# Kernel tuning notes

Measured on AMD Instinct MI355X. Metric: run time of the kernel, lower is better.

## Reference

```python
import jax, jax.numpy as jnp
import numpy as np

B, T, C = 4, 2048, 1024
H = 16
HD = C // H  # 64


def setup_inputs() -> dict:
    key = jax.random.key(0)
    k1, k2, k3 = jax.random.split(key, 3)
    x = jax.random.normal(k1, (B, T, C), dtype=jnp.float32)
    W_attn = jax.random.normal(k2, (C, 3 * C), dtype=jnp.float32) * (1.0 / np.sqrt(C))
    b_attn = jnp.zeros((3 * C,), dtype=jnp.float32)
    W_proj = jax.random.normal(k3, (C, C), dtype=jnp.float32) * (1.0 / np.sqrt(C))
    b_proj = jnp.zeros((C,), dtype=jnp.float32)
    return {"x": x, "W_attn": W_attn, "b_attn": b_attn, "W_proj": W_proj, "b_proj": b_proj}


def reference(x, W_attn, b_attn, W_proj, b_proj):
    Bx, Tx, Cx = x.shape
    qkv = x @ W_attn + b_attn                      # [B,T,3C]
    q, k, v = jnp.split(qkv, 3, axis=-1)
    # [B,T,C] -> [B,H,T,HD]
    q = q.reshape(Bx, Tx, H, HD).transpose(0, 2, 1, 3)
    k = k.reshape(Bx, Tx, H, HD).transpose(0, 2, 1, 3)
    v = v.reshape(Bx, Tx, H, HD).transpose(0, 2, 1, 3)
    att = jnp.einsum('bhqd,bhkd->bhqk', q, k) / jnp.sqrt(jnp.float32(HD))
    causal = jnp.tril(jnp.ones((Tx, Tx), dtype=bool))
    att = jnp.where(causal[None, None], att, -jnp.inf)
    att = jax.nn.softmax(att, axis=-1)
    y = jnp.einsum('bhqk,bhkd->bhqd', att, v)      # [B,H,T,HD]
    y = y.transpose(0, 2, 1, 3).reshape(Bx, Tx, Cx)
    return y @ W_proj + b_proj
```

## Files before the change

### kernel.cpp

```cpp
#include <hip/hip_runtime.h>
#include <hip/hip_bf16.h>

typedef unsigned short u16;
typedef __attribute__((ext_vector_type(8))) short bf16x8;
typedef __attribute__((ext_vector_type(4))) float f32x4;

#define MFMA16(a, b, c) __builtin_amdgcn_mfma_f32_16x16x32_bf16((a), (b), (c), 0, 0, 0)

__device__ __forceinline__ u16 f2bf(float f) {
  union { float f; unsigned u; } v; v.f = f;
  unsigned r = v.u + 0x7fffu + ((v.u >> 16) & 1u);
  return (u16)(r >> 16);
}

__device__ __forceinline__ unsigned pk_trunc(float hi, float lo) {
  union { float f; unsigned u; } a, b; a.f = hi; b.f = lo;
  return __builtin_amdgcn_perm(a.u, b.u, 0x07060302u);
}

__device__ __forceinline__ void gload_lds16(const u16* g, u16* l) {
  __builtin_amdgcn_global_load_lds((const __attribute__((address_space(1))) void*)g,
                                   (__attribute__((address_space(3))) void*)l, 16, 0, 0);
}

__global__ __launch_bounds__(256) void convert_bf16_k(const float* __restrict__ in,
                                                      u16* __restrict__ out, int n) {
  int i = (blockIdx.x * 256 + threadIdx.x) * 4;
  if (i >= n) return;
  float4 v = *(const float4*)(in + i);
  ushort4 o;
  o.x = f2bf(v.x); o.y = f2bf(v.y); o.z = f2bf(v.z); o.w = f2bf(v.w);
  *(ushort4*)(out + i) = o;
}

__global__ __launch_bounds__(256) void transpose2_k(const float* __restrict__ Wa, u16* __restrict__ WaT,
                                                    const float* __restrict__ Wp, u16* __restrict__ WpT) {
  __shared__ float tile[64][65];
  int b = blockIdx.x;
  const float* W; u16* Wt; int N, n0, k0;
  if (b < 768) { W = Wa; Wt = WaT; N = 3072; n0 = (b % 48) * 64; k0 = (b / 48) * 64; }
  else { int c = b - 768; W = Wp; Wt = WpT; N = 1024; n0 = (c & 15) * 64; k0 = (c >> 4) * 64; }
  const int tx = threadIdx.x & 63, ty = threadIdx.x >> 6;
#pragma unroll
  for (int i = 0; i < 16; ++i)
    tile[ty + 4 * i][tx] = W[(size_t)(k0 + ty + 4 * i) * N + n0 + tx];
  __syncthreads();
#pragma unroll
  for (int i = 0; i < 16; ++i)
    Wt[(size_t)(n0 + ty + 4 * i) * 1024 + k0 + tx] = f2bf(tile[tx][ty + 4 * i]);
}

#define GEMM_PROLOG                                                                \
  __shared__ u16 As[128 * 32];                                                     \
  __shared__ u16 Bs[128 * 32];                                                     \
  const int tid = threadIdx.x;                                                     \
  const int w = tid >> 6, lane = tid & 63;                                         \
  const int wm = w & 1, wn = w >> 1;                                               \
  const int fr = lane & 15, fg = lane >> 4;                                        \
  const int srow = lane >> 2, skof = (lane & 3) * 8;                               \
  u16* lA = As + w * 1024;                                                         \
  u16* lB = Bs + w * 1024;                                                         \
  f32x4 acc[4][4];                                                                 \
  _Pragma("unroll") for (int i = 0; i < 4; i++)                                    \
      _Pragma("unroll") for (int j = 0; j < 4; j++) acc[i][j] = (f32x4){0, 0, 0, 0};

#define GEMM_KLOOP(Aptr, Btptr, SWAP)                                              \
  {                                                                                \
    const u16* gA0 = (Aptr) + (size_t)(m0 + w * 32 + srow) * 1024 + skof;          \
    const u16* gB0 = (Btptr) + (size_t)(n0 + w * 32 + srow) * 1024 + skof;         \
    for (int kt = 0; kt < 32; ++kt) {                                              \
      const int ko = kt * 32;                                                      \
      gload_lds16(gA0 + ko, lA);                                                   \
      gload_lds16(gA0 + ko + 16 * 1024, lA + 512);                                 \
      gload_lds16(gB0 + ko, lB);                                                   \
      gload_lds16(gB0 + ko + 16 * 1024, lB + 512);                                 \
      __syncthreads();                                                             \
      bf16x8 af[4], bfr[4];                                                        \
      _Pragma("unroll") for (int mb = 0; mb < 4; ++mb)                             \
          af[mb] = *(const bf16x8*)&As[(wm * 64 + mb * 16 + fr) * 32 + fg * 8];    \
      _Pragma("unroll") for (int nb = 0; nb < 4; ++nb)                             \
          bfr[nb] = *(const bf16x8*)&Bs[(wn * 64 + nb * 16 + fr) * 32 + fg * 8];   \
      _Pragma("unroll") for (int mb = 0; mb < 4; ++mb)                             \
          _Pragma("unroll") for (int nb = 0; nb < 4; ++nb)                         \
              acc[mb][nb] = (SWAP) ? MFMA16(bfr[nb], af[mb], acc[mb][nb])          \
                                   : MFMA16(af[mb], bfr[nb], acc[mb][nb]);         \
      __syncthreads();                                                             \
    }                                                                              \
  }

__global__ __launch_bounds__(256) void gemm_qkv(const u16* __restrict__ A,
                                                const u16* __restrict__ Bt,
                                                const float* __restrict__ bias,
                                                u16* __restrict__ Qo, u16* __restrict__ Ko,
                                                u16* __restrict__ Vt) {
  const int id = blockIdx.x;
  const int s = id >> 3;
  const int nt = (id & 7) * 3 + s % 3;
  const int mt = s / 3;
  const int m0 = mt * 128, n0 = nt * 128;
  GEMM_PROLOG
  const int which = n0 >> 10;
  if (which < 2) {
    GEMM_KLOOP(A, Bt, 1)
    const float sc = (which == 0) ? 0.125f : 1.0f;
    u16* Out = (which == 0) ? Qo : Ko;
#pragma unroll
    for (int mb = 0; mb < 4; ++mb) {
      const int tg = m0 + wm * 64 + mb * 16 + fr;
      const int bb = tg >> 11, t = tg & 2047;
#pragma unroll
      for (int nb = 0; nb < 4; ++nb) {
        const int n = n0 + wn * 64 + nb * 16 + 4 * fg;
        const float4 b4 = *(const float4*)(bias + n);
        const int c = n & 1023, h = c >> 6, d0 = c & 63;
        const float v0 = (acc[mb][nb][0] + b4.x) * sc;
        const float v1 = (acc[mb][nb][1] + b4.y) * sc;
        const float v2 = (acc[mb][nb][2] + b4.z) * sc;
        const float v3 = (acc[mb][nb][3] + b4.w) * sc;
        const unsigned lo = (unsigned)f2bf(v0) | ((unsigned)f2bf(v1) << 16);
        const unsigned hi = (unsigned)f2bf(v2) | ((unsigned)f2bf(v3) << 16);
        *(uint2*)(Out + ((size_t)(bb * 16 + h) * 2048 + t) * 64 + d0) = make_uint2(lo, hi);
      }
    }
  } else {
    GEMM_KLOOP(A, Bt, 0)
#pragma unroll
    for (int nb = 0; nb < 4; ++nb) {
      const int n = n0 + wn * 64 + nb * 16 + fr;
      const float bs = bias[n];
      const int c = n & 1023, h = c >> 6, hd = c & 63;
#pragma unroll
      for (int mb = 0; mb < 4; ++mb) {
        const int mbase = m0 + wm * 64 + mb * 16 + fg * 4;
        const int bb = mbase >> 11, t = mbase & 2047;
        ushort4 pv;
        pv.x = f2bf(acc[mb][nb][0] + bs);
        pv.y = f2bf(acc[mb][nb][1] + bs);
        pv.z = f2bf(acc[mb][nb][2] + bs);
        pv.w = f2bf(acc[mb][nb][3] + bs);
        *(ushort4*)(Vt + ((size_t)(bb * 16 + h) * 64 + hd) * 2048 + t) = pv;
      }
    }
  }
}

__global__ __launch_bounds__(256) void gemm_proj(const u16* __restrict__ A,
                                                 const u16* __restrict__ Bt,
                                                 const float* __restrict__ bias,
                                                 float* __restrict__ O) {
  const int id = blockIdx.x;
  const int m0 = (id >> 3) * 128, n0 = (id & 7) * 128;
  GEMM_PROLOG
  GEMM_KLOOP(A, Bt, 1)
#pragma unroll
  for (int mb = 0; mb < 4; ++mb) {
    const int tg = m0 + wm * 64 + mb * 16 + fr;
#pragma unroll
    for (int nb = 0; nb < 4; ++nb) {
      const int n = n0 + wn * 64 + nb * 16 + 4 * fg;
      const float4 b4 = *(const float4*)(bias + n);
      float4 o;
      o.x = acc[mb][nb][0] + b4.x;
      o.y = acc[mb][nb][1] + b4.y;
      o.z = acc[mb][nb][2] + b4.z;
      o.w = acc[mb][nb][3] + b4.w;
      *(float4*)(O + (size_t)tg * 1024 + n) = o;
    }
  }
}

#define PSTR 72
__global__ __launch_bounds__(256) void attn_k(const u16* __restrict__ Q,
                                              const u16* __restrict__ Kb,
                                              const u16* __restrict__ Vt,
                                              u16* __restrict__ Y) {
  __shared__ u16 Ks[64 * 72];
  __shared__ u16 Vs[64 * 72];
  __shared__ u16 Ps[4 * 32 * PSTR];
  const int L = blockIdx.x;
  const int xcd = L & 7, slot = L >> 3;
  const int bh = xcd * 8 + (slot & 7);
  const int qt = 15 - (slot >> 3);
  const int tid = threadIdx.x, w = tid >> 6, lane = tid & 63;
  const int fr = lane & 15, fg = lane >> 4;
  const u16* Qp = Q + (size_t)bh * 2048 * 64;
  const u16* Kp = Kb + (size_t)bh * 2048 * 64;
  const u16* Vp = Vt + (size_t)bh * 64 * 2048;
  const int qw = qt * 128 + w * 32;

  bf16x8 qa[2][2];
#pragma unroll
  for (int g = 0; g < 2; ++g)
#pragma unroll
    for (int c = 0; c < 2; ++c)
      qa[g][c] = *(const bf16x8*)(Qp + (size_t)(qw + g * 16 + fr) * 64 + c * 32 + fg * 8);

  float li[2] = {0.f, 0.f};
  f32x4 ot[2][4];
#pragma unroll
  for (int g = 0; g < 2; ++g)
#pragma unroll
    for (int mb = 0; mb < 4; ++mb) ot[g][mb] = (f32x4){0, 0, 0, 0};

  const int srow = tid >> 2, scol = (tid & 3) * 16;
  u16* Pw = Ps + w * 32 * PSTR;
  const int nk = 2 * qt + 2;
  const u16* Kg = Kp + (size_t)srow * 64 + scol;
  const u16* Vg = Vp + (size_t)srow * 2048 + scol;

  uint4 kr0 = *(const uint4*)(Kg);
  uint4 kr1 = *(const uint4*)(Kg + 8);
  uint4 vr0 = *(const uint4*)(Vg);
  uint4 vr1 = *(const uint4*)(Vg + 8);

  for (int jt = 0; jt < nk; ++jt) {
    const int k0 = jt * 64;
    if (jt) __syncthreads();
    *(uint4*)&Ks[srow * 72 + scol] = kr0;
    *(uint4*)&Ks[srow * 72 + scol + 8] = kr1;
    *(uint4*)&Vs[srow * 72 + scol] = vr0;
    *(uint4*)&Vs[srow * 72 + scol + 8] = vr1;
    __syncthreads();
    if (jt + 1 < nk) {
      const int kn = (jt + 1) * 64;
      kr0 = *(const uint4*)(Kg + (size_t)kn * 64);
      kr1 = *(const uint4*)(Kg + (size_t)kn * 64 + 8);
      vr0 = *(const uint4*)(Vg + kn);
      vr1 = *(const uint4*)(Vg + kn + 8);
    }
    if (k0 > qw + 31) continue;

    bf16x8 kb[4][2];
#pragma unroll
    for (int nb = 0; nb < 4; ++nb) {
      kb[nb][0] = *(const bf16x8*)&Ks[(nb * 16 + fr) * 72 + fg * 8];
      kb[nb][1] = *(const bf16x8*)&Ks[(nb * 16 + fr) * 72 + 32 + fg * 8];
    }
    f32x4 st[2][4];
#pragma unroll
    for (int g = 0; g < 2; ++g)
#pragma unroll
      for (int nb = 0; nb < 4; ++nb) {
        f32x4 z = (f32x4){0, 0, 0, 0};
        z = MFMA16(kb[nb][0], qa[g][0], z);
        z = MFMA16(kb[nb][1], qa[g][1], z);
        st[g][nb] = z;
      }
    const bool needmask = (k0 + 63 > qw);
#pragma unroll
    for (int g = 0; g < 2; ++g) {
      const int q = qw + g * 16 + fr;
      float rs0 = 0.f, rs1 = 0.f;
#pragma unroll
      for (int nb = 0; nb < 4; ++nb) {
        const int kcb = k0 + nb * 16 + 4 * fg;
        float p0 = __expf(st[g][nb][0]);
        float p1 = __expf(st[g][nb][1]);
        float p2 = __expf(st[g][nb][2]);
        float p3 = __expf(st[g][nb][3]);
        if (needmask) {
          p0 = (kcb + 0 > q) ? 0.f : p0;
          p1 = (kcb + 1 > q) ? 0.f : p1;
          p2 = (kcb + 2 > q) ? 0.f : p2;
          p3 = (kcb + 3 > q) ? 0.f : p3;
        }
        rs0 += p0 + p1;
        rs1 += p2 + p3;
        *(uint2*)&Pw[(g * 16 + fr) * PSTR + nb * 16 + 4 * fg] =
            make_uint2(pk_trunc(p1, p0), pk_trunc(p3, p2));
      }
      li[g] += rs0 + rs1;
    }
    bf16x8 pa[2][2];
#pragma unroll
    for (int g = 0; g < 2; ++g)
#pragma unroll
      for (int H = 0; H < 2; ++H)
        pa[g][H] = *(const bf16x8*)&Pw[(g * 16 + fr) * PSTR + H * 32 + fg * 8];
#pragma unroll
    for (int mb = 0; mb < 4; ++mb) {
      bf16x8 vb0 = *(const bf16x8*)&Vs[(mb * 16 + fr) * 72 + fg * 8];
      bf16x8 vb1 = *(const bf16x8*)&Vs[(mb * 16 + fr) * 72 + 32 + fg * 8];
#pragma unroll
      for (int g = 0; g < 2; ++g) {
        ot[g][mb] = MFMA16(vb0, pa[g][0], ot[g][mb]);
        ot[g][mb] = MFMA16(vb1, pa[g][1], ot[g][mb]);
      }
    }
  }

  const int b = bh >> 4, h = bh & 15;
#pragma unroll
  for (int g = 0; g < 2; ++g) {
    float l = li[g];
    l += __shfl_xor(l, 16);
    l += __shfl_xor(l, 32);
    const float inv = 1.0f / l;
    const int t = qw + g * 16 + fr;
    u16* yrow = Y + ((size_t)b * 2048 + t) * 1024 + h * 64;
#pragma unroll
    for (int mb = 0; mb < 4; ++mb) {
      const unsigned d0 = (unsigned)f2bf(ot[g][mb][0] * inv) |
                          ((unsigned)f2bf(ot[g][mb][1] * inv) << 16);
      const unsigned d1 = (unsigned)f2bf(ot[g][mb][2] * inv) |
                          ((unsigned)f2bf(ot[g][mb][3] * inv) << 16);
      *(uint2*)&yrow[mb * 16 + fg * 4] = make_uint2(d0, d1);
    }
  }
}

extern "C" void kernel_launch(void* const* d_in, const int* in_sizes, int n_in,
                              void* d_out, int out_size, void* d_ws, size_t ws_size,
                              hipStream_t stream) {
  const float* x = (const float*)d_in[0];
  const float* Wa = (const float*)d_in[1];
  const float* ba = (const float*)d_in[2];
  const float* Wp = (const float*)d_in[3];
  const float* bp = (const float*)d_in[4];
  float* out = (float*)d_out;

  char* p = (char*)d_ws;
  u16* xb = (u16*)p;   p += (size_t)8192 * 1024 * 2;
  u16* WaT = (u16*)p;  p += (size_t)3072 * 1024 * 2;
  u16* WpT = (u16*)p;  p += (size_t)1024 * 1024 * 2;
  u16* Qb = (u16*)p;   p += (size_t)64 * 2048 * 64 * 2;
  u16* Kbuf = (u16*)p; p += (size_t)64 * 2048 * 64 * 2;
  u16* Vtb = (u16*)p;  p += (size_t)64 * 64 * 2048 * 2;
  u16* Yb = (u16*)p;   p += (size_t)8192 * 1024 * 2;

  convert_bf16_k<<<8192, 256, 0, stream>>>(x, xb, 8192 * 1024);
  transpose2_k<<<1024, 256, 0, stream>>>(Wa, WaT, Wp, WpT);
  gemm_qkv<<<1536, 256, 0, stream>>>(xb, WaT, ba, Qb, Kbuf, Vtb);
  attn_k<<<1024, 256, 0, stream>>>(Qb, Kbuf, Vtb, Yb);
  gemm_proj<<<512, 256, 0, stream>>>(Yb, WpT, bp, out);
}
```

Measured before the change: 271.7 us.

## Double attention query tile per block and simplify QKV GEMM epilogue and grid

The attention kernel now gives each wave 64 query rows (256 per block) instead of 32, so every K/V tile staged in shared memory is reused across twice as many queries, and the grid is halved to 512 blocks. The QKV GEMM drops the XCD-aware block swizzle in favour of a plain 2D grid, and uses a single non-swapped MFMA order with scalar strided stores for Q and K. The goal is to cut K/V reload traffic and barrier overhead per query. In exchange, register pressure rises (more accumulators), there are fewer blocks for load balance on the causal triangle, and the Q/K stores become uncoalesced 2-byte writes.

```diff
diff --git a/kernel.cpp b/kernel.cpp
--- a/kernel.cpp
+++ b/kernel.cpp
@@ -93,46 +93,29 @@
                                                 const float* __restrict__ bias,
                                                 u16* __restrict__ Qo, u16* __restrict__ Ko,
                                                 u16* __restrict__ Vt) {
-  const int id = blockIdx.x;
-  const int s = id >> 3;
-  const int nt = (id & 7) * 3 + s % 3;
-  const int mt = s / 3;
-  const int m0 = mt * 128, n0 = nt * 128;
+  const int m0 = blockIdx.y * 128, n0 = blockIdx.x * 128;
   GEMM_PROLOG
+  GEMM_KLOOP(A, Bt, 0)
   const int which = n0 >> 10;
-  if (which < 2) {
-    GEMM_KLOOP(A, Bt, 1)
-    const float sc = (which == 0) ? 0.125f : 1.0f;
-    u16* Out = (which == 0) ? Qo : Ko;
+#pragma unroll
+  for (int nb = 0; nb < 4; ++nb) {
+    const int n = n0 + wn * 64 + nb * 16 + fr;
+    const float bs = bias[n];
+    const int c = n & 1023, h = c >> 6, hd = c & 63;
 #pragma unroll
     for (int mb = 0; mb < 4; ++mb) {
-      const int tg = m0 + wm * 64 + mb * 16 + fr;
-      const int bb = tg >> 11, t = tg & 2047;
-#pragma unroll
-      for (int nb = 0; nb < 4; ++nb) {
-        const int n = n0 + wn * 64 + nb * 16 + 4 * fg;
-        const float4 b4 = *(const float4*)(bias + n);
-        const int c = n & 1023, h = c >> 6, d0 = c & 63;
-        const float v0 = (acc[mb][nb][0] + b4.x) * sc;
-        const float v1 = (acc[mb][nb][1] + b4.y) * sc;
-        const float v2 = (acc[mb][nb][2] + b4.z) * sc;
-        const float v3 = (acc[mb][nb][3] + b4.w) * sc;
-        const unsigned lo = (unsigned)f2bf(v0) | ((unsigned)f2bf(v1) << 16);
-        const unsigned hi = (unsigned)f2bf(v2) | ((unsigned)f2bf(v3) << 16);
-        *(uint2*)(Out + ((size_t)(bb * 16 + h) * 2048 + t) * 64 + d0) = make_uint2(lo, hi);
-      }
-    }
-  } else {
-    GEMM_KLOOP(A, Bt, 0)
-#pragma unroll
-    for (int nb = 0; nb < 4; ++nb) {
-      const int n = n0 + wn * 64 + nb * 16 + fr;
-      const float bs = bias[n];
-      const int c = n & 1023, h = c >> 6, hd = c & 63;
-#pragma unroll
-      for (int mb = 0; mb < 4; ++mb) {
-        const int mbase = m0 + wm * 64 + mb * 16 + fg * 4;
-        const int bb = mbase >> 11, t = mbase & 2047;
+      const int mbase = m0 + wm * 64 + mb * 16 + fg * 4;
+      const int bb = mbase >> 11;
+      const int t = mbase & 2047;
+      if (which == 0) {
+        u16* dst = Qo + ((size_t)(bb * 16 + h) * 2048 + t) * 64 + hd;
+#pragma unroll
+        for (int r = 0; r < 4; ++r) dst[(size_t)r * 64] = f2bf((acc[mb][nb][r] + bs) * 0.125f);
+      } else if (which == 1) {
+        u16* dst = Ko + ((size_t)(bb * 16 + h) * 2048 + t) * 64 + hd;
+#pragma unroll
+        for (int r = 0; r < 4; ++r) dst[(size_t)r * 64] = f2bf(acc[mb][nb][r] + bs);
+      } else {
         ushort4 pv;
         pv.x = f2bf(acc[mb][nb][0] + bs);
         pv.y = f2bf(acc[mb][nb][1] + bs);
@@ -176,35 +159,35 @@
                                               u16* __restrict__ Y) {
   __shared__ u16 Ks[64 * 72];
   __shared__ u16 Vs[64 * 72];
-  __shared__ u16 Ps[4 * 32 * PSTR];
+  __shared__ u16 Ps[4 * 64 * PSTR];
   const int L = blockIdx.x;
   const int xcd = L & 7, slot = L >> 3;
   const int bh = xcd * 8 + (slot & 7);
-  const int qt = 15 - (slot >> 3);
+  const int qt = 7 - (slot >> 3);
   const int tid = threadIdx.x, w = tid >> 6, lane = tid & 63;
   const int fr = lane & 15, fg = lane >> 4;
   const u16* Qp = Q + (size_t)bh * 2048 * 64;
   const u16* Kp = Kb + (size_t)bh * 2048 * 64;
   const u16* Vp = Vt + (size_t)bh * 64 * 2048;
-  const int qw = qt * 128 + w * 32;
-
-  bf16x8 qa[2][2];
-#pragma unroll
-  for (int g = 0; g < 2; ++g)
+  const int qw = qt * 256 + w * 64;
+
+  bf16x8 qa[4][2];
+#pragma unroll
+  for (int g = 0; g < 4; ++g)
 #pragma unroll
     for (int c = 0; c < 2; ++c)
       qa[g][c] = *(const bf16x8*)(Qp + (size_t)(qw + g * 16 + fr) * 64 + c * 32 + fg * 8);
 
-  float li[2] = {0.f, 0.f};
-  f32x4 ot[2][4];
-#pragma unroll
-  for (int g = 0; g < 2; ++g)
+  float li[4] = {0.f, 0.f, 0.f, 0.f};
+  f32x4 ot[4][4];
+#pragma unroll
+  for (int g = 0; g < 4; ++g)
 #pragma unroll
     for (int mb = 0; mb < 4; ++mb) ot[g][mb] = (f32x4){0, 0, 0, 0};
 
   const int srow = tid >> 2, scol = (tid & 3) * 16;
-  u16* Pw = Ps + w * 32 * PSTR;
-  const int nk = 2 * qt + 2;
+  u16* Pw = Ps + w * 64 * PSTR;
+  const int nk = 4 * qt + 4;
   const u16* Kg = Kp + (size_t)srow * 64 + scol;
   const u16* Vg = Vp + (size_t)srow * 2048 + scol;
 
@@ -228,7 +211,7 @@
       vr0 = *(const uint4*)(Vg + kn);
       vr1 = *(const uint4*)(Vg + kn + 8);
     }
-    if (k0 > qw + 31) continue;
+    if (k0 > qw + 63) continue;
 
     bf16x8 kb[4][2];
 #pragma unroll
@@ -236,28 +219,26 @@
       kb[nb][0] = *(const bf16x8*)&Ks[(nb * 16 + fr) * 72 + fg * 8];
       kb[nb][1] = *(const bf16x8*)&Ks[(nb * 16 + fr) * 72 + 32 + fg * 8];
     }
-    f32x4 st[2][4];
-#pragma unroll
-    for (int g = 0; g < 2; ++g)
+    const bool needmask = (k0 + 63 > qw);
+#pragma unroll
+    for (int g = 0; g < 4; ++g) {
+      f32x4 st[4];
 #pragma unroll
       for (int nb = 0; nb < 4; ++nb) {
         f32x4 z = (f32x4){0, 0, 0, 0};
         z = MFMA16(kb[nb][0], qa[g][0], z);
         z = MFMA16(kb[nb][1], qa[g][1], z);
-        st[g][nb] = z;
+        st[nb] = z;
       }
-    const bool needmask = (k0 + 63 > qw);
-#pragma unroll
-    for (int g = 0; g < 2; ++g) {
       const int q = qw + g * 16 + fr;
       float rs0 = 0.f, rs1 = 0.f;
 #pragma unroll
       for (int nb = 0; nb < 4; ++nb) {
         const int kcb = k0 + nb * 16 + 4 * fg;
-        float p0 = __expf(st[g][nb][0]);
-        float p1 = __expf(st[g][nb][1]);
-        float p2 = __expf(st[g][nb][2]);
-        float p3 = __expf(st[g][nb][3]);
+        float p0 = __expf(st[nb][0]);
+        float p1 = __expf(st[nb][1]);
+        float p2 = __expf(st[nb][2]);
+        float p3 = __expf(st[nb][3]);
         if (needmask) {
           p0 = (kcb + 0 > q) ? 0.f : p0;
           p1 = (kcb + 1 > q) ? 0.f : p1;
@@ -271,27 +252,27 @@
       }
       li[g] += rs0 + rs1;
     }
-    bf16x8 pa[2][2];
-#pragma unroll
-    for (int g = 0; g < 2; ++g)
-#pragma unroll
-      for (int H = 0; H < 2; ++H)
-        pa[g][H] = *(const bf16x8*)&Pw[(g * 16 + fr) * PSTR + H * 32 + fg * 8];
+    bf16x8 vb[4][2];
 #pragma unroll
     for (int mb = 0; mb < 4; ++mb) {
-      bf16x8 vb0 = *(const bf16x8*)&Vs[(mb * 16 + fr) * 72 + fg * 8];
-      bf16x8 vb1 = *(const bf16x8*)&Vs[(mb * 16 + fr) * 72 + 32 + fg * 8];
-#pragma unroll
-      for (int g = 0; g < 2; ++g) {
-        ot[g][mb] = MFMA16(vb0, pa[g][0], ot[g][mb]);
-        ot[g][mb] = MFMA16(vb1, pa[g][1], ot[g][mb]);
+      vb[mb][0] = *(const bf16x8*)&Vs[(mb * 16 + fr) * 72 + fg * 8];
+      vb[mb][1] = *(const bf16x8*)&Vs[(mb * 16 + fr) * 72 + 32 + fg * 8];
+    }
+#pragma unroll
+    for (int g = 0; g < 4; ++g) {
+      bf16x8 pa0 = *(const bf16x8*)&Pw[(g * 16 + fr) * PSTR + fg * 8];
+      bf16x8 pa1 = *(const bf16x8*)&Pw[(g * 16 + fr) * PSTR + 32 + fg * 8];
+#pragma unroll
+      for (int mb = 0; mb < 4; ++mb) {
+        ot[g][mb] = MFMA16(vb[mb][0], pa0, ot[g][mb]);
+        ot[g][mb] = MFMA16(vb[mb][1], pa1, ot[g][mb]);
       }
     }
   }
 
   const int b = bh >> 4, h = bh & 15;
 #pragma unroll
-  for (int g = 0; g < 2; ++g) {
+  for (int g = 0; g < 4; ++g) {
     float l = li[g];
     l += __shfl_xor(l, 16);
     l += __shfl_xor(l, 32);
@@ -330,7 +311,7 @@
 
   convert_bf16_k<<<8192, 256, 0, stream>>>(x, xb, 8192 * 1024);
   transpose2_k<<<1024, 256, 0, stream>>>(Wa, WaT, Wp, WpT);
-  gemm_qkv<<<1536, 256, 0, stream>>>(xb, WaT, ba, Qb, Kbuf, Vtb);
-  attn_k<<<1024, 256, 0, stream>>>(Qb, Kbuf, Vtb, Yb);
+  gemm_qkv<<<dim3(24, 64), 256, 0, stream>>>(xb, WaT, ba, Qb, Kbuf, Vtb);
+  attn_k<<<512, 256, 0, stream>>>(Qb, Kbuf, Vtb, Yb);
   gemm_proj<<<512, 256, 0, stream>>>(Yb, WpT, bp, out);
 }
```

Result: slower. 285.5 us (+5.1%).
